# Performance work log

Measured on AMD Instinct MI355X. Metric: run time of the kernel, lower is better.

Reference implementation:

```python
import jax, jax.numpy as jnp
import numpy as np

N = 10000      # nodes
E = 160000     # edges
D_IN = 512
D_H = 512
P_DROP = 0.2


def _glorot(key, shape):
    lim = float(np.sqrt(6.0 / (shape[0] + shape[1])))
    return jax.random.uniform(key, shape, jnp.float32, -lim, lim)


def setup_inputs() -> dict:
    key = jax.random.key(0)
    ks = jax.random.split(key, 8)
    h = jax.random.normal(ks[0], (N, D_IN), jnp.float32)
    src = jax.random.randint(ks[1], (E,), 0, N)
    dst = jax.random.randint(ks[2], (E,), 0, N)
    edge_weight = jax.random.uniform(ks[3], (E,), jnp.float32)
    W0 = _glorot(ks[4], (D_IN, D_H))
    W1 = _glorot(ks[5], (D_H, D_H))
    W2 = _glorot(ks[6], (D_H, D_H))
    b0 = jnp.zeros((D_H,), jnp.float32)
    b1 = jnp.zeros((D_H,), jnp.float32)
    b2 = jnp.zeros((D_H,), jnp.float32)
    return dict(h=h, src=src, dst=dst, edge_weight=edge_weight,
                W0=W0, b0=b0, W1=W1, b1=b1, W2=W2, b2=b2)


def _dropout(x, key):
    keep = jax.random.bernoulli(key, 1.0 - P_DROP, x.shape)
    return jnp.where(keep, x / (1.0 - P_DROP), 0.0)


def _graph_conv(x, src, dst, ew, W, b, act):
    # DGL GraphConv, norm='both', weight=True, bias=True, with edge_weight.
    ones = jnp.ones((src.shape[0],), x.dtype)
    deg_out = jnp.maximum(jax.ops.segment_sum(ones, src, num_segments=N), 1.0)
    deg_in = jnp.maximum(jax.ops.segment_sum(ones, dst, num_segments=N), 1.0)
    x = x * (deg_out ** -0.5)[:, None]          # src norm
    msg = x[src] * ew[:, None]                  # [E, D] gather + edge weight
    agg = jax.ops.segment_sum(msg, dst, num_segments=N)  # scatter-add
    out = (agg @ W) * (deg_in ** -0.5)[:, None] + b
    return act(out) if act is not None else out


def reference(h, src, dst, edge_weight, W0, b0, W1, b1, W2, b2):
    dk = jax.random.split(jax.random.key(42), 3)
    x = _dropout(h, dk[0])
    x = _graph_conv(x, src, dst, edge_weight, W0, b0, jax.nn.elu)
    x = _dropout(x, dk[1])
    x = _graph_conv(x, src, dst, edge_weight, W1, b1, jax.nn.elu)
    x = _dropout(x, dk[2])
    x = _graph_conv(x, src, dst, edge_weight, W2, b2, None)
    return x
```

## Files before the change

kernel.cpp:

```cpp
#include <hip/hip_runtime.h>
#include <stdint.h>

#define N_NODES 10000
#define N_EDGES 160000
#define D 512
#define TOT (N_NODES * D)
#define M_PAD 10112

typedef _Float16 h8 __attribute__((ext_vector_type(8)));
typedef float f4 __attribute__((ext_vector_type(4)));

__host__ __device__ inline uint32_t rotl32(uint32_t v, int r) {
    return (v << r) | (v >> (32 - r));
}

__host__ __device__ inline void tf2x32(uint32_t k0, uint32_t k1,
                                       uint32_t& x0, uint32_t& x1) {
    uint32_t k2 = k0 ^ k1 ^ 0x1BD11BDAu;
    x0 += k0; x1 += k1;
    x0 += x1; x1 = rotl32(x1, 13); x1 ^= x0;
    x0 += x1; x1 = rotl32(x1, 15); x1 ^= x0;
    x0 += x1; x1 = rotl32(x1, 26); x1 ^= x0;
    x0 += x1; x1 = rotl32(x1,  6); x1 ^= x0;
    x0 += k1; x1 += k2 + 1u;
    x0 += x1; x1 = rotl32(x1, 17); x1 ^= x0;
    x0 += x1; x1 = rotl32(x1, 29); x1 ^= x0;
    x0 += x1; x1 = rotl32(x1, 16); x1 ^= x0;
    x0 += x1; x1 = rotl32(x1, 24); x1 ^= x0;
    x0 += k2; x1 += k0 + 2u;
    x0 += x1; x1 = rotl32(x1, 13); x1 ^= x0;
    x0 += x1; x1 = rotl32(x1, 15); x1 ^= x0;
    x0 += x1; x1 = rotl32(x1, 26); x1 ^= x0;
    x0 += x1; x1 = rotl32(x1,  6); x1 ^= x0;
    x0 += k0; x1 += k1 + 3u;
    x0 += x1; x1 = rotl32(x1, 17); x1 ^= x0;
    x0 += x1; x1 = rotl32(x1, 29); x1 ^= x0;
    x0 += x1; x1 = rotl32(x1, 16); x1 ^= x0;
    x0 += x1; x1 = rotl32(x1, 24); x1 ^= x0;
    x0 += k1; x1 += k2 + 4u;
    x0 += x1; x1 = rotl32(x1, 13); x1 ^= x0;
    x0 += x1; x1 = rotl32(x1, 15); x1 ^= x0;
    x0 += x1; x1 = rotl32(x1, 26); x1 ^= x0;
    x0 += x1; x1 = rotl32(x1,  6); x1 ^= x0;
    x0 += k2; x1 += k0 + 5u;
}

__device__ __forceinline__ float dropout_gate(uint32_t k0, uint32_t k1, uint32_t j) {
    uint32_t c0 = 0u, c1 = j;
    tf2x32(k0, k1, c0, c1);
    uint32_t bits = c0 ^ c1;
    float u = __uint_as_float((bits >> 9) | 0x3f800000u) - 1.0f;
    return (u < 0.8f) ? 1.0f : 0.0f;
}

__device__ __forceinline__ void gl_lds16(const void* g, void* l) {
    __builtin_amdgcn_global_load_lds(
        (const __attribute__((address_space(1))) void*)g,
        (__attribute__((address_space(3))) void*)l, 16, 0, 0);
}

__global__ void hist_kernel(const int* __restrict__ src, const int* __restrict__ dst,
                            int* __restrict__ deg_out, int* __restrict__ deg_in) {
    int e = blockIdx.x * 256 + threadIdx.x;
    if (e >= N_EDGES) return;
    atomicAdd(&deg_out[src[e]], 1);
    atomicAdd(&deg_in[dst[e]], 1);
}

__global__ __launch_bounds__(1024)
void scan_kernel(const int* __restrict__ deg_in, const int* __restrict__ deg_out,
                 int* __restrict__ row_ptr,
                 float* __restrict__ rn_in, float* __restrict__ rn_out) {
    __shared__ int wsum[16];
    __shared__ int base_s;
    int tid = threadIdx.x;
    int lane = tid & 63, wv = tid >> 6;
    if (tid == 0) base_s = 0;
    __syncthreads();
    for (int start = 0; start < N_NODES; start += 1024) {
        int i = start + tid;
        int v = (i < N_NODES) ? deg_in[i] : 0;
        int s = v;
#pragma unroll
        for (int off = 1; off < 64; off <<= 1) {
            int t = __shfl_up(s, off, 64);
            if (lane >= off) s += t;
        }
        if (lane == 63) wsum[wv] = s;
        __syncthreads();
        if (wv == 0 && lane < 16) {
            int ws = wsum[lane];
#pragma unroll
            for (int off = 1; off < 16; off <<= 1) {
                int t = __shfl_up(ws, off, 64);
                if (lane >= off) ws += t;
            }
            wsum[lane] = ws;
        }
        __syncthreads();
        if (i < N_NODES) {
            int prefix = base_s + ((wv > 0) ? wsum[wv - 1] : 0) + (s - v);
            row_ptr[i] = prefix;
            rn_in[i]  = 1.0f / sqrtf(fmaxf((float)v, 1.0f));
            rn_out[i] = 1.0f / sqrtf(fmaxf((float)deg_out[i], 1.0f));
        }
        __syncthreads();
        if (tid == 0) base_s += wsum[15];
        __syncthreads();
    }
    if (tid == 0) row_ptr[N_NODES] = base_s;
}

__global__ void fill_kernel(const int* __restrict__ src, const int* __restrict__ dst,
                            const float* __restrict__ ew, const int* __restrict__ row_ptr,
                            int* __restrict__ cursor, int2* __restrict__ csr) {
    int e = blockIdx.x * 256 + threadIdx.x;
    if (e >= N_EDGES) return;
    int v = dst[e];
    int pos = atomicAdd(&cursor[v], 1);
    int idx = row_ptr[v] + pos;
    csr[idx] = make_int2(src[e], __float_as_int(ew[e]));
}

__global__ __launch_bounds__(256)
void wconvert_kernel(const float* __restrict__ W0, const float* __restrict__ W1,
                     const float* __restrict__ W2, _Float16* __restrict__ Wt) {
    __shared__ float tile[64][65];
    const float* W = (blockIdx.z == 0) ? W0 : (blockIdx.z == 1) ? W1 : W2;
    _Float16* T = Wt + (size_t)blockIdx.z * 512 * 512;
    int r0 = blockIdx.y * 64, c0 = blockIdx.x * 64;
    int t = threadIdx.x;
    int c = t & 63, rq = t >> 6;
#pragma unroll
    for (int i = 0; i < 16; ++i) {
        int r = rq + i * 4;
        tile[r][c] = W[(size_t)(r0 + r) * 512 + c0 + c];
    }
    __syncthreads();
    int k = t & 63, nq = t >> 6;
#pragma unroll
    for (int i = 0; i < 16; ++i) {
        int n = nq + i * 4;
        T[(size_t)(c0 + n) * 512 + r0 + k] = (_Float16)tile[k][n];
    }
}

__global__ __launch_bounds__(256)
void dropout_kernel(const float* __restrict__ x, _Float16* __restrict__ y,
                    const float* __restrict__ rn_out, uint32_t k0, uint32_t k1) {
    int t = blockIdx.x * 256 + threadIdx.x;
    int j = t * 4;
    if (j >= TOT) return;
    float4 xv = *(const float4*)&x[j];
    float w = rn_out[j >> 9];
    _Float16 r[4];
    uint32_t jj = (uint32_t)j;
#pragma unroll
    for (int i = 0; i < 4; ++i) {
        float g = dropout_gate(k0, k1, jj + (uint32_t)i);
        float xi = (&xv.x)[i];
        r[i] = (_Float16)(g * (xi / 0.8f) * w);
    }
    *(ushort4*)&y[j] = *(ushort4*)r;
}

__global__ __launch_bounds__(256)
void aggregate_kernel(const _Float16* __restrict__ y, const int* __restrict__ row_ptr,
                      const int2* __restrict__ csr, _Float16* __restrict__ agg) {
    int node = blockIdx.x * 4 + (threadIdx.x >> 6);
    int lane = threadIdx.x & 63;
    if (node >= N_NODES) return;
    int beg = row_ptr[node], end = row_ptr[node + 1];
    float acc[8] = {0, 0, 0, 0, 0, 0, 0, 0};
    int k = beg;
    for (; k + 3 < end; k += 4) {
        int2 e0 = csr[k], e1 = csr[k + 1], e2 = csr[k + 2], e3 = csr[k + 3];
        h8 a0 = *(const h8*)&y[(size_t)e0.x * 512 + lane * 8];
        h8 a1 = *(const h8*)&y[(size_t)e1.x * 512 + lane * 8];
        h8 a2 = *(const h8*)&y[(size_t)e2.x * 512 + lane * 8];
        h8 a3 = *(const h8*)&y[(size_t)e3.x * 512 + lane * 8];
        float w0 = __int_as_float(e0.y), w1 = __int_as_float(e1.y);
        float w2 = __int_as_float(e2.y), w3 = __int_as_float(e3.y);
#pragma unroll
        for (int i = 0; i < 8; ++i)
            acc[i] += w0 * (float)a0[i] + w1 * (float)a1[i]
                    + w2 * (float)a2[i] + w3 * (float)a3[i];
    }
    for (; k < end; ++k) {
        int2 e0 = csr[k];
        float w0 = __int_as_float(e0.y);
        h8 a = *(const h8*)&y[(size_t)e0.x * 512 + lane * 8];
#pragma unroll
        for (int i = 0; i < 8; ++i) acc[i] += w0 * (float)a[i];
    }
    _Float16 r[8];
#pragma unroll
    for (int i = 0; i < 8; ++i) r[i] = (_Float16)acc[i];
    *(h8*)&agg[(size_t)node * 512 + lane * 8] = *(h8*)r;
}

#define GBK 64
__global__ __launch_bounds__(256)
void gemm_kernel(const _Float16* __restrict__ A, const _Float16* __restrict__ Wt,
                 const float* __restrict__ bias, const float* __restrict__ rn_in,
                 const float* __restrict__ rn_out,
                 _Float16* __restrict__ yout, float* __restrict__ fout,
                 int mode, uint32_t k0, uint32_t k1) {
    __shared__ _Float16 As[128 * GBK];
    __shared__ _Float16 Bs[64 * GBK];
    int tid = threadIdx.x;
    int wv = tid >> 6, lane = tid & 63;
    int row0 = blockIdx.y * 128, col0 = blockIdx.x * 64;
    int wr = wv >> 1, wc = wv & 1;

    f4 acc[4][2];
#pragma unroll
    for (int i = 0; i < 4; ++i)
#pragma unroll
        for (int j = 0; j < 2; ++j) acc[i][j] = (f4){0.f, 0.f, 0.f, 0.f};

    int srow = lane >> 3;
    int skc = (lane & 7) * 8;
    const _Float16* pa = A + (size_t)(row0 + 32 * wv + srow) * 512 + skc;
    const _Float16* pb = Wt + (size_t)(col0 + 16 * wv + srow) * 512 + skc;
    _Float16* la = &As[(32 * wv) * GBK];
    _Float16* lb = &Bs[(16 * wv) * GBK];

    int kf = (lane >> 4) * 8;
    const _Float16* fa = &As[(wr * 64 + (lane & 15)) * GBK + kf];
    const _Float16* fb = &Bs[(wc * 32 + (lane & 15)) * GBK + kf];

    for (int kk = 0; kk < 512; kk += GBK) {
#pragma unroll
        for (int r = 0; r < 4; ++r)
            gl_lds16(pa + (size_t)r * 8 * 512 + kk, la + (8 * r) * GBK);
#pragma unroll
        for (int r = 0; r < 2; ++r)
            gl_lds16(pb + (size_t)r * 8 * 512 + kk, lb + (8 * r) * GBK);
        __syncthreads();
#pragma unroll
        for (int ks = 0; ks < 2; ++ks) {
            h8 af[4], bf[2];
#pragma unroll
            for (int mt = 0; mt < 4; ++mt)
                af[mt] = *(const h8*)(fa + mt * 16 * GBK + ks * 32);
#pragma unroll
            for (int nt = 0; nt < 2; ++nt)
                bf[nt] = *(const h8*)(fb + nt * 16 * GBK + ks * 32);
#pragma unroll
            for (int mt = 0; mt < 4; ++mt)
#pragma unroll
                for (int nt = 0; nt < 2; ++nt)
                    acc[mt][nt] = __builtin_amdgcn_mfma_f32_16x16x32_f16(
                        af[mt], bf[nt], acc[mt][nt], 0, 0, 0);
        }
        __syncthreads();
    }

    int mbase = row0 + wr * 64;
    int nbase = col0 + wc * 32;
#pragma unroll
    for (int mt = 0; mt < 4; ++mt) {
#pragma unroll
        for (int nt = 0; nt < 2; ++nt) {
            int gr0 = mbase + mt * 16 + (lane >> 4) * 4;
            int gc = nbase + nt * 16 + (lane & 15);
            float bcol = bias[gc];
#pragma unroll
            for (int i = 0; i < 4; ++i) {
                int gr = gr0 + i;
                if (gr >= N_NODES) continue;
                float v = acc[mt][nt][i] * rn_in[gr] + bcol;
                if (mode == 0) {
                    v = (v > 0.f) ? v : expm1f(v);
                    float g = dropout_gate(k0, k1, (uint32_t)(gr * 512 + gc));
                    v = g * (v / 0.8f) * rn_out[gr];
                    yout[(size_t)gr * 512 + gc] = (_Float16)v;
                } else {
                    fout[(size_t)gr * 512 + gc] = v;
                }
            }
        }
    }
}

extern "C" void kernel_launch(void* const* d_in, const int* in_sizes, int n_in,
                              void* d_out, int out_size, void* d_ws, size_t ws_size,
                              hipStream_t stream) {
    const float* h   = (const float*)d_in[0];
    const int*   src = (const int*)d_in[1];
    const int*   dst = (const int*)d_in[2];
    const float* ew  = (const float*)d_in[3];
    const float* W0  = (const float*)d_in[4];
    const float* b0  = (const float*)d_in[5];
    const float* W1  = (const float*)d_in[6];
    const float* b1  = (const float*)d_in[7];
    const float* W2  = (const float*)d_in[8];
    const float* b2  = (const float*)d_in[9];
    const float* bl[3] = {b0, b1, b2};
    float* out = (float*)d_out;

    char* ws = (char*)d_ws;
    _Float16* y16  = (_Float16*)ws; ws += (size_t)TOT * 2;
    _Float16* aggF = (_Float16*)ws; ws += (size_t)M_PAD * 512 * 2;
    _Float16* Wt   = (_Float16*)ws; ws += (size_t)3 * 512 * 512 * 2;
    int* degi_in  = (int*)ws;  ws += N_NODES * 4;
    int* degi_out = (int*)ws;  ws += N_NODES * 4;
    int* cursor   = (int*)ws;  ws += N_NODES * 4;
    int* row_ptr  = (int*)ws;  ws += (N_NODES + 1) * 4;
    ws = (char*)(((uintptr_t)ws + 15) & ~(uintptr_t)15);
    int2* csr     = (int2*)ws; ws += (size_t)N_EDGES * 8;
    float* rn_in  = (float*)ws; ws += N_NODES * 4;
    float* rn_out = (float*)ws; ws += N_NODES * 4;

    hipMemsetAsync(degi_in, 0, 3 * N_NODES * 4, stream);

    hist_kernel<<<(N_EDGES + 255) / 256, 256, 0, stream>>>(src, dst, degi_out, degi_in);
    scan_kernel<<<1, 1024, 0, stream>>>(degi_in, degi_out, row_ptr, rn_in, rn_out);
    fill_kernel<<<(N_EDGES + 255) / 256, 256, 0, stream>>>(src, dst, ew, row_ptr,
                                                           cursor, csr);
    wconvert_kernel<<<dim3(8, 8, 3), 256, 0, stream>>>(W0, W1, W2, Wt);

    uint32_t dk[3][2];
    for (int i = 0; i < 3; ++i) {
        uint32_t c0 = 0u, c1 = (uint32_t)i;
        tf2x32(0u, 42u, c0, c1);
        dk[i][0] = c0; dk[i][1] = c1;
    }

    dropout_kernel<<<(TOT / 4 + 255) / 256, 256, 0, stream>>>(h, y16, rn_out,
                                                              dk[0][0], dk[0][1]);
    for (int l = 0; l < 3; ++l) {
        aggregate_kernel<<<N_NODES / 4, 256, 0, stream>>>(y16, row_ptr, csr, aggF);
        int mode = (l < 2) ? 0 : 1;
        uint32_t dk0 = (l < 2) ? dk[l + 1][0] : 0u;
        uint32_t dk1 = (l < 2) ? dk[l + 1][1] : 0u;
        gemm_kernel<<<dim3(512 / 64, M_PAD / 128), 256, 0, stream>>>(
            aggF, Wt + (size_t)l * 512 * 512, bl[l], rn_in, rn_out,
            y16, out, mode, dk0, dk1);
    }
}
```

Measured before the change: 310.5 us.

## Register-prefetch GEMM tiles with padded LDS and remapped block order

The GEMM drops direct global-to-LDS loads and instead prefetches the next K-slice (now 32 wide) into registers while MFMAs run on the current one. LDS rows are padded to 40 halfs to avoid bank conflicts. Blocks are remapped so that consecutive block IDs cover different column tiles across row groups, which changes L2 locality. The smaller K-tile doubles the number of barriers, and the register staging adds VGPR pressure.

```diff
diff --git a/kernel.cpp b/kernel.cpp
--- a/kernel.cpp
+++ b/kernel.cpp
@@ -53,12 +53,6 @@
     return (u < 0.8f) ? 1.0f : 0.0f;
 }
 
-__device__ __forceinline__ void gl_lds16(const void* g, void* l) {
-    __builtin_amdgcn_global_load_lds(
-        (const __attribute__((address_space(1))) void*)g,
-        (__attribute__((address_space(3))) void*)l, 16, 0, 0);
-}
-
 __global__ void hist_kernel(const int* __restrict__ src, const int* __restrict__ dst,
                             int* __restrict__ deg_out, int* __restrict__ deg_in) {
     int e = blockIdx.x * 256 + threadIdx.x;
@@ -199,18 +193,23 @@
     *(h8*)&agg[(size_t)node * 512 + lane * 8] = *(h8*)r;
 }
 
-#define GBK 64
+#define GBK 32
+#define LDA 40
 __global__ __launch_bounds__(256)
 void gemm_kernel(const _Float16* __restrict__ A, const _Float16* __restrict__ Wt,
                  const float* __restrict__ bias, const float* __restrict__ rn_in,
                  const float* __restrict__ rn_out,
                  _Float16* __restrict__ yout, float* __restrict__ fout,
                  int mode, uint32_t k0, uint32_t k1) {
-    __shared__ _Float16 As[128 * GBK];
-    __shared__ _Float16 Bs[64 * GBK];
+    __shared__ _Float16 As[128 * LDA];
+    __shared__ _Float16 Bs[64 * LDA];
     int tid = threadIdx.x;
     int wv = tid >> 6, lane = tid & 63;
-    int row0 = blockIdx.y * 128, col0 = blockIdx.x * 64;
+
+    int f = blockIdx.x + blockIdx.y * 8;
+    int T = (f & 7) * 79 + (f >> 3);
+    int row0 = (T >> 3) * 128, col0 = (T & 7) * 64;
+
     int wr = wv >> 1, wc = wv & 1;
 
     f4 acc[4][2];
@@ -219,41 +218,44 @@
 #pragma unroll
         for (int j = 0; j < 2; ++j) acc[i][j] = (f4){0.f, 0.f, 0.f, 0.f};
 
-    int srow = lane >> 3;
-    int skc = (lane & 7) * 8;
-    const _Float16* pa = A + (size_t)(row0 + 32 * wv + srow) * 512 + skc;
-    const _Float16* pb = Wt + (size_t)(col0 + 16 * wv + srow) * 512 + skc;
-    _Float16* la = &As[(32 * wv) * GBK];
-    _Float16* lb = &Bs[(16 * wv) * GBK];
+    int srow = tid >> 2;
+    int sseg = (tid & 3) * 8;
+    const _Float16* gA0 = A + (size_t)(row0 + srow) * 512 + sseg;
+    const _Float16* gA1 = gA0 + (size_t)64 * 512;
+    const _Float16* gB  = Wt + (size_t)(col0 + srow) * 512 + sseg;
+    _Float16* wA0 = &As[srow * LDA + sseg];
+    _Float16* wA1 = &As[(64 + srow) * LDA + sseg];
+    _Float16* wB  = &Bs[srow * LDA + sseg];
 
     int kf = (lane >> 4) * 8;
-    const _Float16* fa = &As[(wr * 64 + (lane & 15)) * GBK + kf];
-    const _Float16* fb = &Bs[(wc * 32 + (lane & 15)) * GBK + kf];
+    const _Float16* fa = &As[(wr * 64 + (lane & 15)) * LDA + kf];
+    const _Float16* fb = &Bs[(wc * 32 + (lane & 15)) * LDA + kf];
+
+    h8 ra0 = *(const h8*)gA0;
+    h8 ra1 = *(const h8*)gA1;
+    h8 rb  = *(const h8*)gB;
 
     for (int kk = 0; kk < 512; kk += GBK) {
-#pragma unroll
-        for (int r = 0; r < 4; ++r)
-            gl_lds16(pa + (size_t)r * 8 * 512 + kk, la + (8 * r) * GBK);
-#pragma unroll
-        for (int r = 0; r < 2; ++r)
-            gl_lds16(pb + (size_t)r * 8 * 512 + kk, lb + (8 * r) * GBK);
-        __syncthreads();
-#pragma unroll
-        for (int ks = 0; ks < 2; ++ks) {
-            h8 af[4], bf[2];
-#pragma unroll
-            for (int mt = 0; mt < 4; ++mt)
-                af[mt] = *(const h8*)(fa + mt * 16 * GBK + ks * 32);
+        *(h8*)wA0 = ra0;
+        *(h8*)wA1 = ra1;
+        *(h8*)wB  = rb;
+        __syncthreads();
+        if (kk + GBK < 512) {
+            ra0 = *(const h8*)(gA0 + kk + GBK);
+            ra1 = *(const h8*)(gA1 + kk + GBK);
+            rb  = *(const h8*)(gB  + kk + GBK);
+        }
+        h8 af[4], bf[2];
+#pragma unroll
+        for (int mt = 0; mt < 4; ++mt) af[mt] = *(const h8*)(fa + mt * 16 * LDA);
+#pragma unroll
+        for (int nt = 0; nt < 2; ++nt) bf[nt] = *(const h8*)(fb + nt * 16 * LDA);
+#pragma unroll
+        for (int mt = 0; mt < 4; ++mt)
 #pragma unroll
             for (int nt = 0; nt < 2; ++nt)
-                bf[nt] = *(const h8*)(fb + nt * 16 * GBK + ks * 32);
-#pragma unroll
-            for (int mt = 0; mt < 4; ++mt)
-#pragma unroll
-                for (int nt = 0; nt < 2; ++nt)
-                    acc[mt][nt] = __builtin_amdgcn_mfma_f32_16x16x32_f16(
-                        af[mt], bf[nt], acc[mt][nt], 0, 0, 0);
-        }
+                acc[mt][nt] = __builtin_amdgcn_mfma_f32_16x16x32_f16(
+                    af[mt], bf[nt], acc[mt][nt], 0, 0, 0);
         __syncthreads();
     }
 
@@ -335,7 +337,7 @@
         int mode = (l < 2) ? 0 : 1;
         uint32_t dk0 = (l < 2) ? dk[l + 1][0] : 0u;
         uint32_t dk1 = (l < 2) ? dk[l + 1][1] : 0u;
-        gemm_kernel<<<dim3(512 / 64, M_PAD / 128), 256, 0, stream>>>(
+        gemm_kernel<<<dim3(8, M_PAD / 128), 256, 0, stream>>>(
             aggF, Wt + (size_t)l * 512 * 512, bl[l], rn_in, rn_out,
             y16, out, mode, dk0, dk1);
     }
```

Result: no change. 308.9 us (-0.5%).
